# Optimization experiments

Hardware: AMD Instinct MI355X
Metric: run time of the kernel (lower is better)

## Reference

```python
import jax, jax.numpy as jnp
import numpy as np

N_NODES = 100000
N_EDGES = 1600000
D_IN = 128
D_H = 128
NEG_SLOPE = 0.2  # DGL GATConv default


def gat_layer(x, W, attn_l, attn_r, bias, src, dst, n_nodes):
    # x: [N, Din] -> h: [N, H]  (num_heads=1, head dim squeezed)
    h = x @ W
    el = jnp.einsum('nh,h->n', h, attn_l)  # [N]
    er = jnp.einsum('nh,h->n', h, attn_r)  # [N]
    e = jax.nn.leaky_relu(el[src] + er[dst], NEG_SLOPE)  # [E]
    # edge softmax over incoming edges of each dst node (numerically stable)
    m = jax.ops.segment_max(e, dst, num_segments=n_nodes)  # [N], -inf on zero-in-degree
    ex = jnp.exp(e - m[dst])  # [E]
    s = jax.ops.segment_sum(ex, dst, num_segments=n_nodes)  # [N]
    a = ex / s[dst]  # [E]
    out = jax.ops.segment_sum(a[:, None] * h[src], dst, num_segments=n_nodes)  # [N, H]
    return out + bias


def setup_inputs() -> dict:
    key = jax.random.key(0)
    ks = jax.random.split(key, 16)
    feat = jax.random.normal(ks[0], (N_NODES, D_IN), dtype=jnp.float32)
    src = jax.random.randint(ks[1], (N_EDGES,), 0, N_NODES, dtype=jnp.int32)
    dst = jax.random.randint(ks[2], (N_EDGES,), 0, N_NODES, dtype=jnp.int32)
    def xavier(k, shape):
        fan = sum(shape)
        return jax.random.normal(k, shape, dtype=jnp.float32) * jnp.sqrt(2.0 / fan)
    params = {}
    dims = [D_IN, D_H, D_H]
    for i in range(3):
        params[f'W{i+1}'] = xavier(ks[3 + 4 * i], (dims[i], D_H))
        params[f'al{i+1}'] = xavier(ks[4 + 4 * i], (D_H,))
        params[f'ar{i+1}'] = xavier(ks[5 + 4 * i], (D_H,))
        params[f'b{i+1}'] = jnp.zeros((D_H,), dtype=jnp.float32)
    return dict(feat=feat, src=src, dst=dst, **params)


def reference(feat, src, dst, W1, al1, ar1, b1, W2, al2, ar2, b2, W3, al3, ar3, b3):
    n = feat.shape[0]
    h = gat_layer(feat, W1, al1, ar1, b1, src, dst, n)
    h = gat_layer(h, W2, al2, ar2, b2, src, dst, n)
    h = gat_layer(h, W3, al3, ar3, b3, src, dst, n)
    return h  # [N, H] (head dim of size 1 squeezed)
```

## Files before the change

### kernel.cpp

```cpp
#include <hip/hip_runtime.h>

#define DH 128
#define NBMAX 1024
#define BCH 8192

typedef __attribute__((ext_vector_type(8))) short s16x8;
typedef __attribute__((ext_vector_type(4))) float f32x4;

__device__ __forceinline__ ushort f2bf(float x) {
  uint u = __builtin_bit_cast(uint, x);
  u = (u + 0x7FFF + ((u >> 16) & 1)) >> 16;
  return (ushort)u;
}
__device__ __forceinline__ float bfl2f(uint u) {
  return __builtin_bit_cast(float, u << 16);
}
__device__ __forceinline__ float bfh2f(uint u) {
  return __builtin_bit_cast(float, u & 0xFFFF0000u);
}


__global__ __launch_bounds__(256) void chist_kernel(const int* __restrict__ dst,
                                                    int* __restrict__ chist, int E, int NB) {
  __shared__ int h[NBMAX];
  int t = threadIdx.x;
  for (int i = t; i < NB; i += 256) h[i] = 0;
  __syncthreads();
  int base = blockIdx.x * BCH;
  int n = min(BCH, E - base);
  for (int i = t; i < n; i += 256) atomicAdd(&h[((uint)dst[base + i]) >> 7], 1);
  __syncthreads();
  for (int i = t; i < NB; i += 256)
    if (h[i]) atomicAdd(&chist[i * 16], h[i]);
}

__global__ __launch_bounds__(256) void cscan_kernel(const int* __restrict__ chist,
                                                    int* __restrict__ cbase, int* __restrict__ ccur,
                                                    int* __restrict__ rowptr, int N, int NB, int E) {
  __shared__ int lds[256];
  int t = threadIdx.x;
  int v[4], s = 0;
#pragma unroll
  for (int j = 0; j < 4; ++j) {
    int idx = t * 4 + j;
    v[j] = (idx < NB) ? chist[idx * 16] : 0;
    s += v[j];
  }
  lds[t] = s;
  __syncthreads();
  for (int off = 1; off < 256; off <<= 1) {
    int add = (t >= off) ? lds[t - off] : 0;
    __syncthreads();
    lds[t] += add;
    __syncthreads();
  }
  int run = t ? lds[t - 1] : 0;
#pragma unroll
  for (int j = 0; j < 4; ++j) {
    int idx = t * 4 + j;
    if (idx < NB) {
      cbase[idx] = run;
      ccur[idx * 16] = run;
    }
    run += v[j];
  }
  if (t == 255) cbase[NB] = lds[255];
  if (t == 0) rowptr[N] = E;
}

__global__ __launch_bounds__(256) void binscat_kernel(const int* __restrict__ src,
                                                      const int* __restrict__ dst,
                                                      int* __restrict__ ccur,
                                                      uint* __restrict__ puv, int E, int NB) {
  __shared__ int h[NBMAX];
  __shared__ int gb[NBMAX];
  int t = threadIdx.x;
  int base = blockIdx.x * BCH;
  int n = min(BCH, E - base);
  for (int i = t; i < NB; i += 256) h[i] = 0;
  __syncthreads();
  for (int i = t; i < n; i += 256) atomicAdd(&h[((uint)dst[base + i]) >> 7], 1);
  __syncthreads();
  for (int i = t; i < NB; i += 256) {
    int c = h[i];
    gb[i] = c ? atomicAdd(&ccur[i * 16], c) : 0;
    h[i] = 0;
  }
  __syncthreads();
  for (int i = t; i < n; i += 256) {
    uint d = (uint)dst[base + i];
    int b = d >> 7;
    int p = gb[b] + atomicAdd(&h[b], 1);
    puv[p] = ((d & 127u) << 25) | (uint)src[base + i];
  }
}

__global__ __launch_bounds__(256) void finesort_kernel(const uint* __restrict__ puv,
                                                       const int* __restrict__ cbase,
                                                       int* __restrict__ rowptr,
                                                       int* __restrict__ ssrc, int N) {
  int b = blockIdx.x;
  int base = cbase[b];
  int cnt = cbase[b + 1] - base;
  __shared__ int ncnt[128], nincl[128], noff[128];
  int t = threadIdx.x;
  if (t < 128) ncnt[t] = 0;
  __syncthreads();
  for (int i = t; i < cnt; i += 256) atomicAdd(&ncnt[puv[base + i] >> 25], 1);
  __syncthreads();
  if (t < 128) nincl[t] = ncnt[t];
  __syncthreads();
  for (int off = 1; off < 128; off <<= 1) {
    int add = (t < 128 && t >= off) ? nincl[t - off] : 0;
    __syncthreads();
    if (t < 128) nincl[t] += add;
    __syncthreads();
  }
  if (t < 128) {
    noff[t] = nincl[t] - ncnt[t];
    int node = (b << 7) + t;
    if (node < N) rowptr[node] = base + noff[t];
    ncnt[t] = 0;
  }
  __syncthreads();
  for (int i = t; i < cnt; i += 256) {
    uint e = puv[base + i];
    int ln = e >> 25;
    int p = base + noff[ln] + atomicAdd(&ncnt[ln], 1);
    ssrc[p] = (int)(e & 0x1FFFFFFu);
  }
}

__global__ __launch_bounds__(256) void wt_kernel(const float* __restrict__ W,
                                                 ushort* __restrict__ Wtb) {
  int i = blockIdx.x * 256 + threadIdx.x;
  int col = i >> 7, k = i & 127;
  Wtb[(size_t)col * DH + k] = f2bf(W[(size_t)k * DH + col]);
}

template <bool XF32>
__global__ __launch_bounds__(256) void gemm_kernel(const void* __restrict__ xin,
                                                   const ushort* __restrict__ Wtb,
                                                   const float* __restrict__ al,
                                                   const float* __restrict__ ar,
                                                   ushort* __restrict__ hb,
                                                   float* __restrict__ el,
                                                   float* __restrict__ er, int M) {
  __shared__ ushort As[64 * DH];
  __shared__ ushort Bs[DH * DH];
  int t = threadIdx.x;
  int R0 = blockIdx.x * 64;

  for (int i = t; i < 2048; i += 256) {
    int col = i >> 4, kb = i & 15;
    s16x8 v = *(const s16x8*)(Wtb + (size_t)col * DH + kb * 8);
    *(s16x8*)(&Bs[col * DH + ((kb ^ (col & 15)) * 8)]) = v;
  }
  for (int i = t; i < 1024; i += 256) {
    int row = i >> 4, kb = i & 15;
    int gr = R0 + row;
    s16x8 v;
    if (gr < M) {
      if constexpr (XF32) {
        const float4* p = (const float4*)((const float*)xin + (size_t)gr * DH + kb * 8);
        float4 a = p[0], b = p[1];
        v[0] = (short)f2bf(a.x); v[1] = (short)f2bf(a.y);
        v[2] = (short)f2bf(a.z); v[3] = (short)f2bf(a.w);
        v[4] = (short)f2bf(b.x); v[5] = (short)f2bf(b.y);
        v[6] = (short)f2bf(b.z); v[7] = (short)f2bf(b.w);
      } else {
        v = *(const s16x8*)((const ushort*)xin + (size_t)gr * DH + kb * 8);
      }
    } else {
      v = (s16x8)0;
    }
    *(s16x8*)(&As[row * DH + ((kb ^ (row & 15)) * 8)]) = v;
  }
  __syncthreads();

  int w = t >> 6, lane = t & 63;
  int li = lane & 15, lq = lane >> 4;
  f32x4 acc[8] = {};
  int arow = w * 16 + li;
#pragma unroll
  for (int kc = 0; kc < 4; ++kc) {
    int kb = kc * 4 + lq;
    s16x8 af = *(const s16x8*)(&As[arow * DH + ((kb ^ (arow & 15)) * 8)]);
#pragma unroll
    for (int cf = 0; cf < 8; ++cf) {
      int bcol = cf * 16 + li;
      s16x8 bf = *(const s16x8*)(&Bs[bcol * DH + ((kb ^ (bcol & 15)) * 8)]);
      acc[cf] = __builtin_amdgcn_mfma_f32_16x16x32_bf16(af, bf, acc[cf], 0, 0, 0);
    }
  }

  int Rw = R0 + w * 16;
  float alv[8], arv[8];
#pragma unroll
  for (int cf = 0; cf < 8; ++cf) {
    alv[cf] = al[cf * 16 + li];
    arv[cf] = ar[cf * 16 + li];
  }
#pragma unroll
  for (int r = 0; r < 4; ++r) {
    float sl = 0.f, sr = 0.f;
#pragma unroll
    for (int cf = 0; cf < 8; ++cf) {
      sl += acc[cf][r] * alv[cf];
      sr += acc[cf][r] * arv[cf];
    }
#pragma unroll
    for (int off = 1; off <= 8; off <<= 1) {
      sl += __shfl_xor(sl, off);
      sr += __shfl_xor(sr, off);
    }
    int grow = Rw + lq * 4 + r;
    if (li == 0 && grow < M) {
      el[grow] = sl;
      er[grow] = sr;
    }
  }

  ushort* hl = &As[w * 16 * DH];
#pragma unroll
  for (int cf = 0; cf < 8; ++cf)
#pragma unroll
    for (int r = 0; r < 4; ++r) hl[(lq * 4 + r) * DH + cf * 16 + li] = f2bf(acc[cf][r]);
  __syncthreads();
#pragma unroll
  for (int p = 0; p < 4; ++p) {
    int row = lane >> 2;
    int blk = (lane & 3) + p * 4;
    s16x8 v = *(const s16x8*)(&hl[row * DH + blk * 8]);
    int grow = Rw + row;
    if (grow < M) *(s16x8*)(hb + (size_t)grow * DH + blk * 8) = v;
  }
}

template <int FINAL>
__global__ __launch_bounds__(256) void agg_kernel(const ushort* __restrict__ hb,
                                                  const float* __restrict__ el,
                                                  const float* __restrict__ er,
                                                  const int* __restrict__ rowptr,
                                                  const int* __restrict__ ssrc,
                                                  const float* __restrict__ bias,
                                                  void* __restrict__ outv, int M) {
  int wid = (blockIdx.x * blockDim.x + threadIdx.x) >> 6;
  int lane = threadIdx.x & 63;
  if (wid >= M) return;
  int begin = rowptr[wid], end = rowptr[wid + 1];
  int deg = end - begin;

  if (deg > 64) {
    float er_d = er[wid];
    float mx = -1e30f;
    for (int e = begin + lane; e < end; e += 64) {
      float s = el[ssrc[e]] + er_d;
      s = s > 0.f ? s : 0.2f * s;
      mx = fmaxf(mx, s);
    }
#pragma unroll
    for (int off = 32; off; off >>= 1) mx = fmaxf(mx, __shfl_xor(mx, off));
    float acc0 = 0.f, acc1 = 0.f, ssum_l = 0.f;
    for (int base = begin; base < end; base += 64) {
      int n = min(64, end - base);
      int e = base + lane;
      int idx = 0;
      float wgt = 0.f;
      if (lane < n) {
        idx = ssrc[e];
        float sc = el[idx] + er_d;
        sc = sc > 0.f ? sc : 0.2f * sc;
        wgt = __expf(sc - mx);
      }
      ssum_l += wgt;
      for (int j = 0; j < n; ++j) {
        int s = __shfl(idx, j);
        float wg = __shfl(wgt, j);
        uint u = ((const uint*)(hb + (size_t)s * DH))[lane];
        acc0 += wg * bfl2f(u);
        acc1 += wg * bfh2f(u);
      }
    }
#pragma unroll
    for (int off = 32; off; off >>= 1) ssum_l += __shfl_xor(ssum_l, off);
    float inv = 1.f / ssum_l;
    float2 b2 = ((const float2*)bias)[lane];
    float o0 = acc0 * inv + b2.x;
    float o1 = acc1 * inv + b2.y;
    if constexpr (FINAL) {
      ((float2*)((float*)outv + (size_t)wid * DH))[lane] = make_float2(o0, o1);
    } else {
      uint p = (uint)f2bf(o0) | ((uint)f2bf(o1) << 16);
      ((uint*)((ushort*)outv + (size_t)wid * DH))[lane] = p;
    }
    return;
  }

  float acc[8] = {};
  float inv = 0.f;
  if (deg > 0) {
    int e = begin + lane;
    int idx = (e < end) ? ssrc[e] : 0;
    float sc = -1e30f;
    if (e < end) {
      sc = el[idx] + er[wid];
      sc = sc > 0.f ? sc : 0.2f * sc;
    }
    float mx = sc;
#pragma unroll
    for (int off = 32; off; off >>= 1) mx = fmaxf(mx, __shfl_xor(mx, off));
    float wgt = (e < end) ? __expf(sc - mx) : 0.f;
    float ssum = wgt;
#pragma unroll
    for (int off = 32; off; off >>= 1) ssum += __shfl_xor(ssum, off);
    inv = 1.f / ssum;

    int q = lane >> 4, cl = lane & 15;
    const uint4* hb4 = (const uint4*)hb;
    for (int j = 0; j < deg; j += 16) {
      uint4 u[4];
      float wq[4];
#pragma unroll
      for (int k = 0; k < 4; ++k) {
        int ej = j + k * 4 + q;
        int s = __shfl(idx, ej);
        wq[k] = __shfl(wgt, ej);
        u[k] = hb4[(size_t)s * 16 + cl];
      }
#pragma unroll
      for (int k = 0; k < 4; ++k) {
        acc[0] += wq[k] * bfl2f(u[k].x); acc[1] += wq[k] * bfh2f(u[k].x);
        acc[2] += wq[k] * bfl2f(u[k].y); acc[3] += wq[k] * bfh2f(u[k].y);
        acc[4] += wq[k] * bfl2f(u[k].z); acc[5] += wq[k] * bfh2f(u[k].z);
        acc[6] += wq[k] * bfl2f(u[k].w); acc[7] += wq[k] * bfh2f(u[k].w);
      }
    }
#pragma unroll
    for (int i = 0; i < 8; ++i) {
      acc[i] += __shfl_xor(acc[i], 16);
      acc[i] += __shfl_xor(acc[i], 32);
    }
  }
  if (lane < 16) {
    float4 b0 = ((const float4*)bias)[lane * 2];
    float4 b1 = ((const float4*)bias)[lane * 2 + 1];
    float o[8];
    o[0] = acc[0] * inv + b0.x; o[1] = acc[1] * inv + b0.y;
    o[2] = acc[2] * inv + b0.z; o[3] = acc[3] * inv + b0.w;
    o[4] = acc[4] * inv + b1.x; o[5] = acc[5] * inv + b1.y;
    o[6] = acc[6] * inv + b1.z; o[7] = acc[7] * inv + b1.w;
    if constexpr (FINAL) {
      float* op = (float*)outv + (size_t)wid * DH + lane * 8;
      *(float4*)op = make_float4(o[0], o[1], o[2], o[3]);
      *(float4*)(op + 4) = make_float4(o[4], o[5], o[6], o[7]);
    } else {
      uint4 p;
      p.x = (uint)f2bf(o[0]) | ((uint)f2bf(o[1]) << 16);
      p.y = (uint)f2bf(o[2]) | ((uint)f2bf(o[3]) << 16);
      p.z = (uint)f2bf(o[4]) | ((uint)f2bf(o[5]) << 16);
      p.w = (uint)f2bf(o[6]) | ((uint)f2bf(o[7]) << 16);
      ((uint4*)((ushort*)outv + (size_t)wid * DH))[lane] = p;
    }
  }
}

extern "C" void kernel_launch(void* const* d_in, const int* in_sizes, int n_in,
                              void* d_out, int out_size, void* d_ws, size_t ws_size,
                              hipStream_t stream) {
  const float* feat = (const float*)d_in[0];
  const int* src = (const int*)d_in[1];
  const int* dst = (const int*)d_in[2];
  const int N = in_sizes[0] / DH;
  const int E = in_sizes[1];
  const int NB = (N + 127) >> 7;
  const float* W[3]  = {(const float*)d_in[3], (const float*)d_in[7],  (const float*)d_in[11]};
  const float* al[3] = {(const float*)d_in[4], (const float*)d_in[8],  (const float*)d_in[12]};
  const float* ar[3] = {(const float*)d_in[5], (const float*)d_in[9],  (const float*)d_in[13]};
  const float* bi[3] = {(const float*)d_in[6], (const float*)d_in[10], (const float*)d_in[14]};

  char* ws = (char*)d_ws;
  size_t off = 0;
  auto alloc = [&](size_t bytes) {
    void* p = ws + off;
    off = (off + bytes + 255) & ~(size_t)255;
    return p;
  };
  ushort* hb   = (ushort*)alloc((size_t)N * DH * sizeof(ushort));
  ushort* xb   = (ushort*)alloc((size_t)N * DH * sizeof(ushort));
  float* el    = (float*)alloc((size_t)N * sizeof(float));
  float* er    = (float*)alloc((size_t)N * sizeof(float));
  int* rowptr  = (int*)alloc((size_t)(N + 1) * sizeof(int));
  int* ssrc    = (int*)alloc((size_t)E * sizeof(int));
  ushort* Wtb  = (ushort*)alloc((size_t)DH * DH * sizeof(ushort));
  int* chist   = (int*)alloc((size_t)NBMAX * 16 * sizeof(int));
  int* cbase   = (int*)alloc((size_t)(NBMAX + 1) * sizeof(int));
  int* ccur    = (int*)alloc((size_t)NBMAX * 16 * sizeof(int));
  uint* puv    = (uint*)hb;

  hipMemsetAsync(chist, 0, (size_t)NBMAX * 16 * sizeof(int), stream);
  int ebl = (E + BCH - 1) / BCH;
  chist_kernel<<<ebl, 256, 0, stream>>>(dst, chist, E, NB);
  cscan_kernel<<<1, 256, 0, stream>>>(chist, cbase, ccur, rowptr, N, NB, E);
  binscat_kernel<<<ebl, 256, 0, stream>>>(src, dst, ccur, puv, E, NB);
  finesort_kernel<<<NB, 256, 0, stream>>>(puv, cbase, rowptr, ssrc, N);

  for (int l = 0; l < 3; ++l) {
    wt_kernel<<<64, 256, 0, stream>>>(W[l], Wtb);
    if (l == 0)
      gemm_kernel<true><<<(N + 63) / 64, 256, 0, stream>>>(feat, Wtb, al[l], ar[l], hb, el, er, N);
    else
      gemm_kernel<false><<<(N + 63) / 64, 256, 0, stream>>>(xb, Wtb, al[l], ar[l], hb, el, er, N);
    if (l < 2)
      agg_kernel<0><<<(N + 3) / 4, 256, 0, stream>>>(hb, el, er, rowptr, ssrc, bi[l], xb, N);
    else
      agg_kernel<1><<<(N + 3) / 4, 256, 0, stream>>>(hb, el, er, rowptr, ssrc, bi[l], d_out, N);
  }
}
```

Measured before the change: 341.0 us.

## Batch weight transposes, enlarge GEMM tiles, use nontemporal stores, bigger bin chunks

Transposes all three layer weights in one launch before the layer loop, removing two launches. Doubles the GEMM row tile to 128 with 512 threads and drops the barrier before the per-wave write-out, since each wave only reads its own slice of shared memory. Writes h and intermediate activations with nontemporal stores and doubles the edge chunk size for the binning kernels. Risks include lower GEMM occupancy from the larger shared-memory footprint and fewer blocks for the histogram and scatter passes.

New measurement: 345.4 us. Within noise of the previous version (+1.3%).

```diff
diff --git a/kernel.cpp b/kernel.cpp
--- a/kernel.cpp
+++ b/kernel.cpp
@@ -2,10 +2,11 @@
 
 #define DH 128
 #define NBMAX 1024
-#define BCH 8192
+#define BCH 16384
 
 typedef __attribute__((ext_vector_type(8))) short s16x8;
 typedef __attribute__((ext_vector_type(4))) float f32x4;
+typedef __attribute__((ext_vector_type(4))) uint u32x4;
 
 __device__ __forceinline__ ushort f2bf(float x) {
   uint u = __builtin_bit_cast(uint, x);
@@ -131,32 +132,37 @@
   }
 }
 
-__global__ __launch_bounds__(256) void wt_kernel(const float* __restrict__ W,
+__global__ __launch_bounds__(256) void wt_kernel(const float* __restrict__ W0,
+                                                 const float* __restrict__ W1,
+                                                 const float* __restrict__ W2,
                                                  ushort* __restrict__ Wtb) {
-  int i = blockIdx.x * 256 + threadIdx.x;
+  int b = blockIdx.x;
+  int layer = b >> 6;
+  const float* W = layer == 0 ? W0 : (layer == 1 ? W1 : W2);
+  int i = (b & 63) * 256 + threadIdx.x;
   int col = i >> 7, k = i & 127;
-  Wtb[(size_t)col * DH + k] = f2bf(W[(size_t)k * DH + col]);
+  Wtb[(size_t)layer * DH * DH + (size_t)col * DH + k] = f2bf(W[(size_t)k * DH + col]);
 }
 
 template <bool XF32>
-__global__ __launch_bounds__(256) void gemm_kernel(const void* __restrict__ xin,
+__global__ __launch_bounds__(512) void gemm_kernel(const void* __restrict__ xin,
                                                    const ushort* __restrict__ Wtb,
                                                    const float* __restrict__ al,
                                                    const float* __restrict__ ar,
                                                    ushort* __restrict__ hb,
                                                    float* __restrict__ el,
                                                    float* __restrict__ er, int M) {
-  __shared__ ushort As[64 * DH];
+  __shared__ ushort As[128 * DH];
   __shared__ ushort Bs[DH * DH];
   int t = threadIdx.x;
-  int R0 = blockIdx.x * 64;
-
-  for (int i = t; i < 2048; i += 256) {
+  int R0 = blockIdx.x * 128;
+
+  for (int i = t; i < 2048; i += 512) {
     int col = i >> 4, kb = i & 15;
     s16x8 v = *(const s16x8*)(Wtb + (size_t)col * DH + kb * 8);
     *(s16x8*)(&Bs[col * DH + ((kb ^ (col & 15)) * 8)]) = v;
   }
-  for (int i = t; i < 1024; i += 256) {
+  for (int i = t; i < 2048; i += 512) {
     int row = i >> 4, kb = i & 15;
     int gr = R0 + row;
     s16x8 v;
@@ -226,14 +232,14 @@
   for (int cf = 0; cf < 8; ++cf)
 #pragma unroll
     for (int r = 0; r < 4; ++r) hl[(lq * 4 + r) * DH + cf * 16 + li] = f2bf(acc[cf][r]);
-  __syncthreads();
 #pragma unroll
   for (int p = 0; p < 4; ++p) {
     int row = lane >> 2;
     int blk = (lane & 3) + p * 4;
     s16x8 v = *(const s16x8*)(&hl[row * DH + blk * 8]);
     int grow = Rw + row;
-    if (grow < M) *(s16x8*)(hb + (size_t)grow * DH + blk * 8) = v;
+    if (grow < M)
+      __builtin_nontemporal_store(v, (s16x8*)(hb + (size_t)grow * DH + blk * 8));
   }
 }
 
@@ -351,16 +357,18 @@
     o[4] = acc[4] * inv + b1.x; o[5] = acc[5] * inv + b1.y;
     o[6] = acc[6] * inv + b1.z; o[7] = acc[7] * inv + b1.w;
     if constexpr (FINAL) {
+      f32x4 p0 = {o[0], o[1], o[2], o[3]};
+      f32x4 p1 = {o[4], o[5], o[6], o[7]};
       float* op = (float*)outv + (size_t)wid * DH + lane * 8;
-      *(float4*)op = make_float4(o[0], o[1], o[2], o[3]);
-      *(float4*)(op + 4) = make_float4(o[4], o[5], o[6], o[7]);
+      *(f32x4*)op = p0;
+      *(f32x4*)(op + 4) = p1;
     } else {
-      uint4 p;
+      u32x4 p;
       p.x = (uint)f2bf(o[0]) | ((uint)f2bf(o[1]) << 16);
       p.y = (uint)f2bf(o[2]) | ((uint)f2bf(o[3]) << 16);
       p.z = (uint)f2bf(o[4]) | ((uint)f2bf(o[5]) << 16);
       p.w = (uint)f2bf(o[6]) | ((uint)f2bf(o[7]) << 16);
-      ((uint4*)((ushort*)outv + (size_t)wid * DH))[lane] = p;
+      __builtin_nontemporal_store(p, (u32x4*)((ushort*)outv + (size_t)wid * DH) + lane);
     }
   }
 }
@@ -392,7 +400,7 @@
   float* er    = (float*)alloc((size_t)N * sizeof(float));
   int* rowptr  = (int*)alloc((size_t)(N + 1) * sizeof(int));
   int* ssrc    = (int*)alloc((size_t)E * sizeof(int));
-  ushort* Wtb  = (ushort*)alloc((size_t)DH * DH * sizeof(ushort));
+  ushort* Wtb  = (ushort*)alloc((size_t)3 * DH * DH * sizeof(ushort));
   int* chist   = (int*)alloc((size_t)NBMAX * 16 * sizeof(int));
   int* cbase   = (int*)alloc((size_t)(NBMAX + 1) * sizeof(int));
   int* ccur    = (int*)alloc((size_t)NBMAX * 16 * sizeof(int));
@@ -404,13 +412,14 @@
   cscan_kernel<<<1, 256, 0, stream>>>(chist, cbase, ccur, rowptr, N, NB, E);
   binscat_kernel<<<ebl, 256, 0, stream>>>(src, dst, ccur, puv, E, NB);
   finesort_kernel<<<NB, 256, 0, stream>>>(puv, cbase, rowptr, ssrc, N);
+  wt_kernel<<<192, 256, 0, stream>>>(W[0], W[1], W[2], Wtb);
 
   for (int l = 0; l < 3; ++l) {
-    wt_kernel<<<64, 256, 0, stream>>>(W[l], Wtb);
+    const ushort* Wl = Wtb + (size_t)l * DH * DH;
     if (l == 0)
-      gemm_kernel<true><<<(N + 63) / 64, 256, 0, stream>>>(feat, Wtb, al[l], ar[l], hb, el, er, N);
+      gemm_kernel<true><<<(N + 127) / 128, 512, 0, stream>>>(feat, Wl, al[l], ar[l], hb, el, er, N);
     else
-      gemm_kernel<false><<<(N + 63) / 64, 256, 0, stream>>>(xb, Wtb, al[l], ar[l], hb, el, er, N);
+      gemm_kernel<false><<<(N + 127) / 128, 512, 0, stream>>>(xb, Wl, al[l], ar[l], hb, el, er, N);
     if (l < 2)
       agg_kernel<0><<<(N + 3) / 4, 256, 0, stream>>>(hb, el, er, rowptr, ssrc, bi[l], xb, N);
     else
```
